# Kernel optimization log

Measured on AMD Instinct MI355X. Metric: run time of the kernel, lower is better.

Reference implementation:

```python
import jax, jax.numpy as jnp
import numpy as np

EPS = 1e-5  # nn.BatchNorm2d default eps
K = 3       # number of adjacency subsets


def setup_inputs() -> dict:
    key = jax.random.key(0)
    ks = jax.random.split(key, 8)
    N, C, T, V = 64, 64, 256, 25
    Cout = 64
    x = jax.random.normal(ks[0], (N, C, T, V), dtype=jnp.float32)
    A = jax.random.uniform(ks[1], (K, V, V), dtype=jnp.float32) * 0.1  # normalized-ish adjacency
    PA = jnp.ones((K, V, V), dtype=jnp.float32)  # torch.ones_like(A) init
    Wc = jax.random.normal(ks[2], (K * Cout, C), dtype=jnp.float32) * 0.05  # 1x1 conv weight
    bc = jax.random.normal(ks[3], (K * Cout,), dtype=jnp.float32) * 0.01
    gamma = 0.5 + jax.random.uniform(ks[4], (Cout,), dtype=jnp.float32)
    beta = jax.random.normal(ks[5], (Cout,), dtype=jnp.float32) * 0.1
    mean = jax.random.normal(ks[6], (Cout,), dtype=jnp.float32) * 0.1
    var = 0.5 + jax.random.uniform(ks[7], (Cout,), dtype=jnp.float32)
    return {"x": x, "A": A, "PA": PA, "Wc": Wc, "bc": bc,
            "gamma": gamma, "beta": beta, "mean": mean, "var": var}


def reference(x, A, PA, Wc, bc, gamma, beta, mean, var):
    # x: (n, c, t, v). in_channels == out_channels -> residual is identity.
    n, c, t, v = x.shape
    res = x
    Aeff = A * PA  # (k, v, w)
    # 1x1 conv: (n,c,t,v) x (o,c) -> (n,o,t,v), o = K*Cout
    y = jnp.einsum('nctv,oc->notv', x, Wc) + bc[None, :, None, None]
    cout = y.shape[1] // K
    y = y.reshape(n, K, cout, t, v)
    # per-subset graph aggregation: (n,k,c,t,v) x (k,v,w) -> (n,c,t,w)
    z = jnp.einsum('nkctv,kvw->nctw', y, Aeff)
    # BatchNorm2d (eval mode) over channel dim
    inv = jax.lax.rsqrt(var + EPS)
    bn = (z - mean[None, :, None, None]) * (gamma * inv)[None, :, None, None] + beta[None, :, None, None]
    return jax.nn.relu(bn + res)
```

## Files before the change

### kernel.cpp

```cpp
#include <hip/hip_runtime.h>
#include <hip/hip_bf16.h>

typedef __attribute__((ext_vector_type(8))) short short8;
typedef __attribute__((ext_vector_type(4))) float floatx4;
typedef __attribute__((ext_vector_type(4))) unsigned short ushortx4;

#define TT 4
#define XS_PITCH 136

#define WS_W2 0
#define WS_AE 24576
#define WS_F  30720
#define WS_S  38912

__device__ __forceinline__ float bf2f(unsigned short u) {
    return __uint_as_float(((unsigned int)u) << 16);
}
__device__ __forceinline__ unsigned short f2bf(float f) {
    unsigned int xx = __float_as_uint(f);
    return (unsigned short)((xx + 0x7fffu + ((xx >> 16) & 1u)) >> 16);
}

__global__ __launch_bounds__(256) void gcn_prep(
    const float* __restrict__ A, const float* __restrict__ PA,
    const float* __restrict__ Wc, const float* __restrict__ bc,
    const float* __restrict__ gamma_, const float* __restrict__ beta_,
    const float* __restrict__ mean_, const float* __restrict__ var_,
    unsigned short* __restrict__ w2, unsigned short* __restrict__ ae,
    float* __restrict__ Fx, float* __restrict__ sarr)
{
    const int b = blockIdx.x, tid = threadIdx.x;
    if (b == 0) {
        __shared__ float cs[96];
        if (tid < 96) {
            int k = tid >> 5, w = tid & 31;
            float s = 0.f;
            if (w < 25)
                for (int v = 0; v < 25; ++v) {
                    int ai = (k * 25 + v) * 25 + w;
                    s += A[ai] * PA[ai];
                }
            cs[tid] = s;
        }
        if (tid < 64) sarr[tid] = gamma_[tid] * rsqrtf(var_[tid] + 1e-5f);
        __syncthreads();
        for (int e = tid; e < 2048; e += 256) {
            int w = e >> 6, co = e & 63;
            float val = 0.f;
            if (w < 25) {
                float sc = gamma_[co] * rsqrtf(var_[co] + 1e-5f);
                val = beta_[co] - mean_[co] * sc
                    + sc * (bc[co] * cs[w] + bc[64 + co] * cs[32 + w] + bc[128 + co] * cs[64 + w]);
            }
            Fx[e] = val;
        }
    } else if (b == 1) {
        for (int e = tid; e < 3072; e += 256) {
            int k = e >> 10, r = e & 1023, w = r >> 5, v = r & 31;
            unsigned short val = 0;
            if (v < 25 && w < 25) {
                int ai = (k * 25 + v) * 25 + w;
                val = f2bf(A[ai] * PA[ai]);
            }
            ae[e] = val;
        }
    } else {
        const int half = b - 2;
        for (int e = tid + half * 6144; e < (half + 1) * 6144; e += 256) {
            int co = e / 192, kc = e % 192, k = kc >> 6, c = kc & 63;
            w2[e] = f2bf(Wc[(k * 64 + co) * 64 + c]);
        }
    }
}

__global__ __launch_bounds__(256, 4) void gcn_main(
    const float* __restrict__ x,
    const unsigned short* __restrict__ w2g,
    const unsigned short* __restrict__ aeg,
    const float* __restrict__ Fg,
    const float* __restrict__ sg,
    float* __restrict__ out)
{
#if defined(__gfx950__)
    __shared__ __align__(16) unsigned short Xs[64 * XS_PITCH];
    __shared__ __align__(16) unsigned short XAbuf[4 * 2 * 1024];

    const int tid = threadIdx.x;
    const int n  = blockIdx.x >> 6;
    const int t0 = (blockIdx.x & 63) * TT;
    const float* xn = x + (size_t)n * 409600;

    {
        const int c = tid >> 2, tl = tid & 3;
        const float* gp = xn + (c * 256 + t0 + tl) * 25;
        unsigned short* dst = &Xs[c * XS_PITCH + tl * 32];
        float f[32];
#pragma unroll
        for (int j = 0; j < 25; ++j) f[j] = gp[j];
#pragma unroll
        for (int j = 25; j < 32; ++j) f[j] = 0.f;
#pragma unroll
        for (int vc = 0; vc < 4; ++vc) {
            union { short8 v; unsigned short s[8]; } u;
#pragma unroll
            for (int j = 0; j < 8; ++j) u.s[j] = f2bf(f[vc * 8 + j]);
            *(short8*)&dst[vc * 8] = u.v;
        }
    }

    const int wave = tid >> 6, lane = tid & 63;
    const int l15 = lane & 15, quad = lane >> 4;
    const int t = wave;

    short8 aeffB[3][2];
#pragma unroll
    for (int k = 0; k < 3; ++k)
#pragma unroll
        for (int nt = 0; nt < 2; ++nt)
            aeffB[k][nt] = *(const short8*)&aeg[(k * 32 + nt * 16 + l15) * 32 + quad * 8];

    __syncthreads();

    unsigned short* xa = &XAbuf[wave * 2048];
    const int wlo3 = l15 & 3, qh = quad >> 1, ql = quad & 1;
    const int woff00 = (l15     ) * 64 + (((0 + qh) ^ wlo3) << 4) + ql * 8;
    const int woff01 = (16 + l15) * 64 + (((0 + qh) ^ wlo3) << 4) + ql * 8;
    const int woff10 = (l15     ) * 64 + (((2 + qh) ^ wlo3) << 4) + ql * 8;
    const int woff11 = (16 + l15) * 64 + (((2 + qh) ^ wlo3) << 4) + ql * 8;
    const int roff0  = (l15     ) * 64 + ((quad ^ wlo3) << 4);
    const int roff1  = (16 + l15) * 64 + ((quad ^ wlo3) << 4);

    const floatx4 zero4 = {0.f, 0.f, 0.f, 0.f};
    floatx4 zacc[4][2];
#pragma unroll
    for (int ct = 0; ct < 4; ++ct) { zacc[ct][0] = zero4; zacc[ct][1] = zero4; }

    const unsigned short* xsrow = &Xs[t * 32 + quad * 8];

#pragma unroll
    for (int ch = 0; ch < 6; ++ch) {
        const int k = ch >> 1, cc = ch & 1;
        char* xab = (char*)xa + (ch & 1) * 2048;

        short8 xf0 = *(const short8*)&xsrow[(cc * 32      + l15) * XS_PITCH];
        short8 xf1 = *(const short8*)&xsrow[(cc * 32 + 16 + l15) * XS_PITCH];
        floatx4 d00 = __builtin_amdgcn_mfma_f32_16x16x32_bf16(xf0, aeffB[k][0], zero4, 0, 0, 0);
        floatx4 d01 = __builtin_amdgcn_mfma_f32_16x16x32_bf16(xf0, aeffB[k][1], zero4, 0, 0, 0);
        floatx4 d10 = __builtin_amdgcn_mfma_f32_16x16x32_bf16(xf1, aeffB[k][0], zero4, 0, 0, 0);
        floatx4 d11 = __builtin_amdgcn_mfma_f32_16x16x32_bf16(xf1, aeffB[k][1], zero4, 0, 0, 0);

        {
            ushortx4 p;
            p[0] = f2bf(d00[0]); p[1] = f2bf(d00[1]); p[2] = f2bf(d00[2]); p[3] = f2bf(d00[3]);
            *(ushortx4*)(xab + woff00) = p;
            p[0] = f2bf(d01[0]); p[1] = f2bf(d01[1]); p[2] = f2bf(d01[2]); p[3] = f2bf(d01[3]);
            *(ushortx4*)(xab + woff01) = p;
            p[0] = f2bf(d10[0]); p[1] = f2bf(d10[1]); p[2] = f2bf(d10[2]); p[3] = f2bf(d10[3]);
            *(ushortx4*)(xab + woff10) = p;
            p[0] = f2bf(d11[0]); p[1] = f2bf(d11[1]); p[2] = f2bf(d11[2]); p[3] = f2bf(d11[3]);
            *(ushortx4*)(xab + woff11) = p;
        }

        short8 b0 = *(const short8*)(xab + roff0);
        short8 b1 = *(const short8*)(xab + roff1);
        const unsigned short* wrow = &w2g[l15 * 192 + k * 64 + cc * 32 + quad * 8];
#pragma unroll
        for (int ct = 0; ct < 4; ++ct) {
            short8 wf = *(const short8*)&wrow[ct * 16 * 192];
            zacc[ct][0] = __builtin_amdgcn_mfma_f32_16x16x32_bf16(wf, b0, zacc[ct][0], 0, 0, 0);
            zacc[ct][1] = __builtin_amdgcn_mfma_f32_16x16x32_bf16(wf, b1, zacc[ct][1], 0, 0, 0);
        }
    }

    const unsigned short* resp = &Xs[(quad * 4) * XS_PITCH + t * 32 + l15];
    float* outp = out + ((size_t)(n * 64 + quad * 4) * 256 + t0 + t) * 25 + l15;
#pragma unroll
    for (int ct = 0; ct < 4; ++ct) {
        floatx4 sv = *(const floatx4*)&sg[ct * 16 + quad * 4];
#pragma unroll
        for (int wt = 0; wt < 2; ++wt) {
            floatx4 Fv = *(const floatx4*)&Fg[(wt * 16 + l15) * 64 + ct * 16 + quad * 4];
            if (wt == 0 || l15 < 9) {
#pragma unroll
                for (int r = 0; r < 4; ++r) {
                    float xres = bf2f(resp[(ct * 16 + r) * XS_PITCH + wt * 16]);
                    float val = sv[r] * zacc[ct][wt][r] + Fv[r] + xres;
                    outp[(size_t)(ct * 16 + r) * 6400 + wt * 16] = fmaxf(val, 0.f);
                }
            }
        }
    }
#else
    (void)x; (void)w2g; (void)aeg; (void)Fg; (void)sg; (void)out;
#endif
}

extern "C" void kernel_launch(void* const* d_in, const int* in_sizes, int n_in,
                              void* d_out, int out_size, void* d_ws, size_t ws_size,
                              hipStream_t stream) {
    (void)in_sizes; (void)n_in; (void)out_size; (void)ws_size;
    unsigned short* w2 = (unsigned short*)((char*)d_ws + WS_W2);
    unsigned short* ae = (unsigned short*)((char*)d_ws + WS_AE);
    float*          Fx = (float*)((char*)d_ws + WS_F);
    float*          sa = (float*)((char*)d_ws + WS_S);

    gcn_prep<<<dim3(4), dim3(256), 0, stream>>>(
        (const float*)d_in[1], (const float*)d_in[2], (const float*)d_in[3],
        (const float*)d_in[4], (const float*)d_in[5], (const float*)d_in[6],
        (const float*)d_in[7], (const float*)d_in[8], w2, ae, Fx, sa);

    gcn_main<<<dim3(64 * 64), dim3(256), 0, stream>>>(
        (const float*)d_in[0], w2, ae, Fx, sa, (float*)d_out);
}
```

Measured before the change: 270.8 us.

## Process eight timesteps per block with XOR-swizzled LDS and per-output-column passes

Each block now covers 8 timesteps instead of 4, with each wave handling two timesteps, and the grid is halved. The X tile is stored in LDS with an XOR swizzle instead of padding. The output-vertex tiles (wt) are processed sequentially, so only one set of Aeff fragments and two accumulator sets live at once. The goal is to amortise weight and Aeff loads across more timesteps and cut register pressure, at the cost of fewer blocks, more LDS per block (which may lower occupancy), and a serial loop over wt.

```diff
diff --git a/kernel.cpp b/kernel.cpp
--- a/kernel.cpp
+++ b/kernel.cpp
@@ -4,9 +4,6 @@
 typedef __attribute__((ext_vector_type(8))) short short8;
 typedef __attribute__((ext_vector_type(4))) float floatx4;
 typedef __attribute__((ext_vector_type(4))) unsigned short ushortx4;
-
-#define TT 4
-#define XS_PITCH 136
 
 #define WS_W2 0
 #define WS_AE 24576
@@ -82,110 +79,116 @@
     float* __restrict__ out)
 {
 #if defined(__gfx950__)
-    __shared__ __align__(16) unsigned short Xs[64 * XS_PITCH];
-    __shared__ __align__(16) unsigned short XAbuf[4 * 2 * 1024];
+    __shared__ __align__(16) unsigned short Xs[64 * 256];
+    __shared__ __align__(16) unsigned short XAbuf[8 * 512];
 
     const int tid = threadIdx.x;
-    const int n  = blockIdx.x >> 6;
-    const int t0 = (blockIdx.x & 63) * TT;
+    const int n  = blockIdx.x >> 5;
+    const int t0 = (blockIdx.x & 31) * 8;
     const float* xn = x + (size_t)n * 409600;
 
-    {
-        const int c = tid >> 2, tl = tid & 3;
-        const float* gp = xn + (c * 256 + t0 + tl) * 25;
-        unsigned short* dst = &Xs[c * XS_PITCH + tl * 32];
+#pragma unroll
+    for (int i = 0; i < 2; ++i) {
+        const int idx = tid + i * 256;
+        const int c = idx >> 3, t = idx & 7;
+        const float* gp = xn + (c * 256 + t0 + t) * 25;
         float f[32];
 #pragma unroll
         for (int j = 0; j < 25; ++j) f[j] = gp[j];
 #pragma unroll
         for (int j = 25; j < 32; ++j) f[j] = 0.f;
+        unsigned short* base = &Xs[c * 256];
+        const int sw = c & 7;
 #pragma unroll
         for (int vc = 0; vc < 4; ++vc) {
             union { short8 v; unsigned short s[8]; } u;
 #pragma unroll
             for (int j = 0; j < 8; ++j) u.s[j] = f2bf(f[vc * 8 + j]);
-            *(short8*)&dst[vc * 8] = u.v;
+            *(short8*)&base[(((t * 4 + vc) ^ sw)) * 8] = u.v;
         }
     }
+    __syncthreads();
 
     const int wave = tid >> 6, lane = tid & 63;
     const int l15 = lane & 15, quad = lane >> 4;
-    const int t = wave;
-
-    short8 aeffB[3][2];
-#pragma unroll
-    for (int k = 0; k < 3; ++k)
-#pragma unroll
-        for (int nt = 0; nt < 2; ++nt)
-            aeffB[k][nt] = *(const short8*)&aeg[(k * 32 + nt * 16 + l15) * 32 + quad * 8];
-
-    __syncthreads();
-
-    unsigned short* xa = &XAbuf[wave * 2048];
+    const int tA = wave * 2, tB = wave * 2 + 1;
+    const int swf = l15 & 7;
+
+    unsigned short* bufA = &XAbuf[(wave * 2 + 0) * 512];
+    unsigned short* bufB = &XAbuf[(wave * 2 + 1) * 512];
     const int wlo3 = l15 & 3, qh = quad >> 1, ql = quad & 1;
-    const int woff00 = (l15     ) * 64 + (((0 + qh) ^ wlo3) << 4) + ql * 8;
-    const int woff01 = (16 + l15) * 64 + (((0 + qh) ^ wlo3) << 4) + ql * 8;
-    const int woff10 = (l15     ) * 64 + (((2 + qh) ^ wlo3) << 4) + ql * 8;
-    const int woff11 = (16 + l15) * 64 + (((2 + qh) ^ wlo3) << 4) + ql * 8;
-    const int roff0  = (l15     ) * 64 + ((quad ^ wlo3) << 4);
-    const int roff1  = (16 + l15) * 64 + ((quad ^ wlo3) << 4);
+    const int woff0 = l15 * 32 + ((qh ^ wlo3) << 3) + (ql << 2);
+    const int woff1 = l15 * 32 + (((2 + qh) ^ wlo3) << 3) + (ql << 2);
+    const int roff  = l15 * 32 + ((quad ^ wlo3) << 3);
 
     const floatx4 zero4 = {0.f, 0.f, 0.f, 0.f};
-    floatx4 zacc[4][2];
-#pragma unroll
-    for (int ct = 0; ct < 4; ++ct) { zacc[ct][0] = zero4; zacc[ct][1] = zero4; }
-
-    const unsigned short* xsrow = &Xs[t * 32 + quad * 8];
-
-#pragma unroll
-    for (int ch = 0; ch < 6; ++ch) {
-        const int k = ch >> 1, cc = ch & 1;
-        char* xab = (char*)xa + (ch & 1) * 2048;
-
-        short8 xf0 = *(const short8*)&xsrow[(cc * 32      + l15) * XS_PITCH];
-        short8 xf1 = *(const short8*)&xsrow[(cc * 32 + 16 + l15) * XS_PITCH];
-        floatx4 d00 = __builtin_amdgcn_mfma_f32_16x16x32_bf16(xf0, aeffB[k][0], zero4, 0, 0, 0);
-        floatx4 d01 = __builtin_amdgcn_mfma_f32_16x16x32_bf16(xf0, aeffB[k][1], zero4, 0, 0, 0);
-        floatx4 d10 = __builtin_amdgcn_mfma_f32_16x16x32_bf16(xf1, aeffB[k][0], zero4, 0, 0, 0);
-        floatx4 d11 = __builtin_amdgcn_mfma_f32_16x16x32_bf16(xf1, aeffB[k][1], zero4, 0, 0, 0);
-
-        {
-            ushortx4 p;
-            p[0] = f2bf(d00[0]); p[1] = f2bf(d00[1]); p[2] = f2bf(d00[2]); p[3] = f2bf(d00[3]);
-            *(ushortx4*)(xab + woff00) = p;
-            p[0] = f2bf(d01[0]); p[1] = f2bf(d01[1]); p[2] = f2bf(d01[2]); p[3] = f2bf(d01[3]);
-            *(ushortx4*)(xab + woff01) = p;
-            p[0] = f2bf(d10[0]); p[1] = f2bf(d10[1]); p[2] = f2bf(d10[2]); p[3] = f2bf(d10[3]);
-            *(ushortx4*)(xab + woff10) = p;
-            p[0] = f2bf(d11[0]); p[1] = f2bf(d11[1]); p[2] = f2bf(d11[2]); p[3] = f2bf(d11[3]);
-            *(ushortx4*)(xab + woff11) = p;
-        }
-
-        short8 b0 = *(const short8*)(xab + roff0);
-        short8 b1 = *(const short8*)(xab + roff1);
-        const unsigned short* wrow = &w2g[l15 * 192 + k * 64 + cc * 32 + quad * 8];
-#pragma unroll
-        for (int ct = 0; ct < 4; ++ct) {
-            short8 wf = *(const short8*)&wrow[ct * 16 * 192];
-            zacc[ct][0] = __builtin_amdgcn_mfma_f32_16x16x32_bf16(wf, b0, zacc[ct][0], 0, 0, 0);
-            zacc[ct][1] = __builtin_amdgcn_mfma_f32_16x16x32_bf16(wf, b1, zacc[ct][1], 0, 0, 0);
-        }
-    }
-
-    const unsigned short* resp = &Xs[(quad * 4) * XS_PITCH + t * 32 + l15];
-    float* outp = out + ((size_t)(n * 64 + quad * 4) * 256 + t0 + t) * 25 + l15;
-#pragma unroll
-    for (int ct = 0; ct < 4; ++ct) {
-        floatx4 sv = *(const floatx4*)&sg[ct * 16 + quad * 4];
-#pragma unroll
-        for (int wt = 0; wt < 2; ++wt) {
-            floatx4 Fv = *(const floatx4*)&Fg[(wt * 16 + l15) * 64 + ct * 16 + quad * 4];
-            if (wt == 0 || l15 < 9) {
-#pragma unroll
-                for (int r = 0; r < 4; ++r) {
-                    float xres = bf2f(resp[(ct * 16 + r) * XS_PITCH + wt * 16]);
-                    float val = sv[r] * zacc[ct][wt][r] + Fv[r] + xres;
-                    outp[(size_t)(ct * 16 + r) * 6400 + wt * 16] = fmaxf(val, 0.f);
+
+#pragma unroll 1
+    for (int wt = 0; wt < 2; ++wt) {
+        short8 aeff[3];
+#pragma unroll
+        for (int k = 0; k < 3; ++k)
+            aeff[k] = *(const short8*)&aeg[(k * 32 + wt * 16 + l15) * 32 + quad * 8];
+
+        floatx4 zA[4], zB[4];
+#pragma unroll
+        for (int ct = 0; ct < 4; ++ct) { zA[ct] = zero4; zB[ct] = zero4; }
+
+#pragma unroll
+        for (int ch = 0; ch < 6; ++ch) {
+            const int k = ch >> 1, cc = ch & 1;
+            const int c0 = cc * 32 + l15, c1 = cc * 32 + 16 + l15;
+
+            short8 x0A = *(const short8*)&Xs[c0 * 256 + ((tA * 4 + quad) ^ swf) * 8];
+            short8 x1A = *(const short8*)&Xs[c1 * 256 + ((tA * 4 + quad) ^ swf) * 8];
+            short8 x0B = *(const short8*)&Xs[c0 * 256 + ((tB * 4 + quad) ^ swf) * 8];
+            short8 x1B = *(const short8*)&Xs[c1 * 256 + ((tB * 4 + quad) ^ swf) * 8];
+            floatx4 dA0 = __builtin_amdgcn_mfma_f32_16x16x32_bf16(x0A, aeff[k], zero4, 0, 0, 0);
+            floatx4 dA1 = __builtin_amdgcn_mfma_f32_16x16x32_bf16(x1A, aeff[k], zero4, 0, 0, 0);
+            floatx4 dB0 = __builtin_amdgcn_mfma_f32_16x16x32_bf16(x0B, aeff[k], zero4, 0, 0, 0);
+            floatx4 dB1 = __builtin_amdgcn_mfma_f32_16x16x32_bf16(x1B, aeff[k], zero4, 0, 0, 0);
+
+            {
+                ushortx4 p;
+                p[0] = f2bf(dA0[0]); p[1] = f2bf(dA0[1]); p[2] = f2bf(dA0[2]); p[3] = f2bf(dA0[3]);
+                *(ushortx4*)&bufA[woff0] = p;
+                p[0] = f2bf(dA1[0]); p[1] = f2bf(dA1[1]); p[2] = f2bf(dA1[2]); p[3] = f2bf(dA1[3]);
+                *(ushortx4*)&bufA[woff1] = p;
+                p[0] = f2bf(dB0[0]); p[1] = f2bf(dB0[1]); p[2] = f2bf(dB0[2]); p[3] = f2bf(dB0[3]);
+                *(ushortx4*)&bufB[woff0] = p;
+                p[0] = f2bf(dB1[0]); p[1] = f2bf(dB1[1]); p[2] = f2bf(dB1[2]); p[3] = f2bf(dB1[3]);
+                *(ushortx4*)&bufB[woff1] = p;
+            }
+
+            short8 bA = *(const short8*)&bufA[roff];
+            short8 bB = *(const short8*)&bufB[roff];
+
+            const unsigned short* wrow = &w2g[l15 * 192 + k * 64 + cc * 32 + quad * 8];
+#pragma unroll
+            for (int ct = 0; ct < 4; ++ct) {
+                short8 wf = *(const short8*)&wrow[ct * 16 * 192];
+                zA[ct] = __builtin_amdgcn_mfma_f32_16x16x32_bf16(wf, bA, zA[ct], 0, 0, 0);
+                zB[ct] = __builtin_amdgcn_mfma_f32_16x16x32_bf16(wf, bB, zB[ct], 0, 0, 0);
+            }
+        }
+
+        const int w = wt * 16 + l15;
+        if (wt == 0 || l15 < 9) {
+#pragma unroll
+            for (int tc = 0; tc < 2; ++tc) {
+                const int t = (tc == 0) ? tA : tB;
+                const floatx4* z = (tc == 0) ? zA : zB;
+#pragma unroll
+                for (int ct = 0; ct < 4; ++ct) {
+                    floatx4 sv = *(const floatx4*)&sg[ct * 16 + quad * 4];
+                    floatx4 Fv = *(const floatx4*)&Fg[w * 64 + ct * 16 + quad * 4];
+#pragma unroll
+                    for (int r = 0; r < 4; ++r) {
+                        const int co = ct * 16 + quad * 4 + r;
+                        float xres = bf2f(Xs[co * 256 + (((t * 4 + (w >> 3)) ^ (co & 7)) * 8) + (w & 7)]);
+                        float val = sv[r] * z[ct][r] + Fv[r] + xres;
+                        out[((size_t)(n * 64 + co) * 256 + t0 + t) * 25 + w] = fmaxf(val, 0.f);
+                    }
                 }
             }
         }
@@ -209,6 +212,6 @@
         (const float*)d_in[4], (const float*)d_in[5], (const float*)d_in[6],
         (const float*)d_in[7], (const float*)d_in[8], w2, ae, Fx, sa);
 
-    gcn_main<<<dim3(64 * 64), dim3(256), 0, stream>>>(
+    gcn_main<<<dim3(64 * 32), dim3(256), 0, stream>>>(
         (const float*)d_in[0], w2, ae, Fx, sa, (float*)d_out);
 }
```

New measurement: 422.7 us. 56.1% more time.

## Stage x via coalesced float4 loads and cache W2 in LDS with swizzle

Applied to the files above, without the earlier changes.

The input tile is first loaded with coalesced float4 reads into an LDS staging area, then converted to bf16 into an XOR-swizzled layout that replaces the padded pitch. The conv weight matrix W2 is copied into padded LDS once per block instead of being read from global memory inside the MFMA loop. The per-wave XA buffer becomes single-buffered and reuses the staging region. LDS use rises to about 49KB and launch bounds drop to 3 blocks per SM, which may reduce occupancy and adds two extra barriers.

```diff
diff --git a/kernel.cpp b/kernel.cpp
--- a/kernel.cpp
+++ b/kernel.cpp
@@ -4,9 +4,6 @@
 typedef __attribute__((ext_vector_type(8))) short short8;
 typedef __attribute__((ext_vector_type(4))) float floatx4;
 typedef __attribute__((ext_vector_type(4))) unsigned short ushortx4;
-
-#define TT 4
-#define XS_PITCH 136
 
 #define WS_W2 0
 #define WS_AE 24576
@@ -73,7 +70,7 @@
     }
 }
 
-__global__ __launch_bounds__(256, 4) void gcn_main(
+__global__ __launch_bounds__(256, 3) void gcn_main(
     const float* __restrict__ x,
     const unsigned short* __restrict__ w2g,
     const unsigned short* __restrict__ aeg,
@@ -82,21 +79,43 @@
     float* __restrict__ out)
 {
 #if defined(__gfx950__)
-    __shared__ __align__(16) unsigned short Xs[64 * XS_PITCH];
-    __shared__ __align__(16) unsigned short XAbuf[4 * 2 * 1024];
+    __shared__ __align__(16) unsigned char LB[50176];
+    unsigned short* Xs  = (unsigned short*)LB;
+    unsigned short* XA  = (unsigned short*)(LB + 16384);
+    unsigned short* W2s = (unsigned short*)(LB + 24576);
+    float*          T   = (float*)(LB + 16384);
 
     const int tid = threadIdx.x;
     const int n  = blockIdx.x >> 6;
-    const int t0 = (blockIdx.x & 63) * TT;
+    const int t0 = (blockIdx.x & 63) * 4;
     const float* xn = x + (size_t)n * 409600;
 
+    const int wave = tid >> 6, lane = tid & 63;
+    const int l15 = lane & 15, quad = lane >> 4;
+
+    short8 aeff[3][2];
+#pragma unroll
+    for (int k = 0; k < 3; ++k)
+#pragma unroll
+        for (int nt = 0; nt < 2; ++nt)
+            aeff[k][nt] = *(const short8*)&aeg[(k * 32 + nt * 16 + l15) * 32 + quad * 8];
+
+#pragma unroll
+    for (int i = 0; i < 7; ++i) {
+        int q = tid + (i << 8);
+        if (q < 1600) {
+            int c = q / 25, j = q % 25;
+            *(floatx4*)&T[q * 4] = *(const floatx4*)&xn[c * 6400 + t0 * 25 + j * 4];
+        }
+    }
+    __syncthreads();
+
     {
-        const int c = tid >> 2, tl = tid & 3;
-        const float* gp = xn + (c * 256 + t0 + tl) * 25;
-        unsigned short* dst = &Xs[c * XS_PITCH + tl * 32];
+        const int c = tid >> 2, tl = tid & 3, key = c & 7;
+        const float* tr = &T[c * 100 + tl * 25];
         float f[32];
 #pragma unroll
-        for (int j = 0; j < 25; ++j) f[j] = gp[j];
+        for (int j = 0; j < 25; ++j) f[j] = tr[j];
 #pragma unroll
         for (int j = 25; j < 32; ++j) f[j] = 0.f;
 #pragma unroll
@@ -104,50 +123,48 @@
             union { short8 v; unsigned short s[8]; } u;
 #pragma unroll
             for (int j = 0; j < 8; ++j) u.s[j] = f2bf(f[vc * 8 + j]);
-            *(short8*)&dst[vc * 8] = u.v;
-        }
-    }
-
-    const int wave = tid >> 6, lane = tid & 63;
-    const int l15 = lane & 15, quad = lane >> 4;
+            *(short8*)&Xs[c * 128 + (((tl * 4 + vc) ^ key) << 3)] = u.v;
+        }
+    }
+    __syncthreads();
+
+    {
+        const int co = tid >> 2, g = tid & 3;
+#pragma unroll
+        for (int jj = 0; jj < 6; ++jj) {
+            int j = g * 6 + jj;
+            *(short8*)&W2s[co * 200 + j * 8] = *(const short8*)&w2g[co * 192 + j * 8];
+        }
+    }
+    __syncthreads();
+
     const int t = wave;
-
-    short8 aeffB[3][2];
-#pragma unroll
-    for (int k = 0; k < 3; ++k)
-#pragma unroll
-        for (int nt = 0; nt < 2; ++nt)
-            aeffB[k][nt] = *(const short8*)&aeg[(k * 32 + nt * 16 + l15) * 32 + quad * 8];
-
-    __syncthreads();
-
-    unsigned short* xa = &XAbuf[wave * 2048];
+    char* xab = (char*)XA + wave * 2048;
     const int wlo3 = l15 & 3, qh = quad >> 1, ql = quad & 1;
-    const int woff00 = (l15     ) * 64 + (((0 + qh) ^ wlo3) << 4) + ql * 8;
-    const int woff01 = (16 + l15) * 64 + (((0 + qh) ^ wlo3) << 4) + ql * 8;
-    const int woff10 = (l15     ) * 64 + (((2 + qh) ^ wlo3) << 4) + ql * 8;
+    const int woff00 = l15 * 64        + ((qh ^ wlo3) << 4) + ql * 8;
+    const int woff01 = (16 + l15) * 64 + ((qh ^ wlo3) << 4) + ql * 8;
+    const int woff10 = l15 * 64        + (((2 + qh) ^ wlo3) << 4) + ql * 8;
     const int woff11 = (16 + l15) * 64 + (((2 + qh) ^ wlo3) << 4) + ql * 8;
-    const int roff0  = (l15     ) * 64 + ((quad ^ wlo3) << 4);
+    const int roff0  = l15 * 64        + ((quad ^ wlo3) << 4);
     const int roff1  = (16 + l15) * 64 + ((quad ^ wlo3) << 4);
+    const int xoffX  = ((t * 4 + quad) ^ (l15 & 7)) << 3;
 
     const floatx4 zero4 = {0.f, 0.f, 0.f, 0.f};
     floatx4 zacc[4][2];
 #pragma unroll
     for (int ct = 0; ct < 4; ++ct) { zacc[ct][0] = zero4; zacc[ct][1] = zero4; }
 
-    const unsigned short* xsrow = &Xs[t * 32 + quad * 8];
-
 #pragma unroll
     for (int ch = 0; ch < 6; ++ch) {
         const int k = ch >> 1, cc = ch & 1;
-        char* xab = (char*)xa + (ch & 1) * 2048;
-
-        short8 xf0 = *(const short8*)&xsrow[(cc * 32      + l15) * XS_PITCH];
-        short8 xf1 = *(const short8*)&xsrow[(cc * 32 + 16 + l15) * XS_PITCH];
-        floatx4 d00 = __builtin_amdgcn_mfma_f32_16x16x32_bf16(xf0, aeffB[k][0], zero4, 0, 0, 0);
-        floatx4 d01 = __builtin_amdgcn_mfma_f32_16x16x32_bf16(xf0, aeffB[k][1], zero4, 0, 0, 0);
-        floatx4 d10 = __builtin_amdgcn_mfma_f32_16x16x32_bf16(xf1, aeffB[k][0], zero4, 0, 0, 0);
-        floatx4 d11 = __builtin_amdgcn_mfma_f32_16x16x32_bf16(xf1, aeffB[k][1], zero4, 0, 0, 0);
+        const int c0 = cc * 32 + l15, c1 = c0 + 16;
+
+        short8 xf0 = *(const short8*)&Xs[c0 * 128 + xoffX];
+        short8 xf1 = *(const short8*)&Xs[c1 * 128 + xoffX];
+        floatx4 d00 = __builtin_amdgcn_mfma_f32_16x16x32_bf16(xf0, aeff[k][0], zero4, 0, 0, 0);
+        floatx4 d01 = __builtin_amdgcn_mfma_f32_16x16x32_bf16(xf0, aeff[k][1], zero4, 0, 0, 0);
+        floatx4 d10 = __builtin_amdgcn_mfma_f32_16x16x32_bf16(xf1, aeff[k][0], zero4, 0, 0, 0);
+        floatx4 d11 = __builtin_amdgcn_mfma_f32_16x16x32_bf16(xf1, aeff[k][1], zero4, 0, 0, 0);
 
         {
             ushortx4 p;
@@ -160,32 +177,31 @@
             p[0] = f2bf(d11[0]); p[1] = f2bf(d11[1]); p[2] = f2bf(d11[2]); p[3] = f2bf(d11[3]);
             *(ushortx4*)(xab + woff11) = p;
         }
-
         short8 b0 = *(const short8*)(xab + roff0);
         short8 b1 = *(const short8*)(xab + roff1);
-        const unsigned short* wrow = &w2g[l15 * 192 + k * 64 + cc * 32 + quad * 8];
+
 #pragma unroll
         for (int ct = 0; ct < 4; ++ct) {
-            short8 wf = *(const short8*)&wrow[ct * 16 * 192];
+            short8 wf = *(const short8*)&W2s[(ct * 16 + l15) * 200 + (k * 8 + cc * 4 + quad) * 8];
             zacc[ct][0] = __builtin_amdgcn_mfma_f32_16x16x32_bf16(wf, b0, zacc[ct][0], 0, 0, 0);
             zacc[ct][1] = __builtin_amdgcn_mfma_f32_16x16x32_bf16(wf, b1, zacc[ct][1], 0, 0, 0);
         }
     }
 
-    const unsigned short* resp = &Xs[(quad * 4) * XS_PITCH + t * 32 + l15];
-    float* outp = out + ((size_t)(n * 64 + quad * 4) * 256 + t0 + t) * 25 + l15;
-#pragma unroll
-    for (int ct = 0; ct < 4; ++ct) {
-        floatx4 sv = *(const floatx4*)&sg[ct * 16 + quad * 4];
-#pragma unroll
-        for (int wt = 0; wt < 2; ++wt) {
-            floatx4 Fv = *(const floatx4*)&Fg[(wt * 16 + l15) * 64 + ct * 16 + quad * 4];
-            if (wt == 0 || l15 < 9) {
+#pragma unroll
+    for (int wt = 0; wt < 2; ++wt) {
+        const int w = wt * 16 + l15;
+        if (wt == 0 || l15 < 9) {
+#pragma unroll
+            for (int ct = 0; ct < 4; ++ct) {
+                floatx4 sv = *(const floatx4*)&sg[ct * 16 + quad * 4];
+                floatx4 Fv = *(const floatx4*)&Fg[w * 64 + ct * 16 + quad * 4];
 #pragma unroll
                 for (int r = 0; r < 4; ++r) {
-                    float xres = bf2f(resp[(ct * 16 + r) * XS_PITCH + wt * 16]);
+                    const int co = ct * 16 + quad * 4 + r;
+                    float xres = bf2f(Xs[co * 128 + (((t * 4 + (w >> 3)) ^ (co & 7)) << 3) + (w & 7)]);
                     float val = sv[r] * zacc[ct][wt][r] + Fv[r] + xres;
-                    outp[(size_t)(ct * 16 + r) * 6400 + wt * 16] = fmaxf(val, 0.f);
+                    out[((size_t)(n * 64 + co) * 256 + t0 + t) * 25 + w] = fmaxf(val, 0.f);
                 }
             }
         }
```

New measurement: 252.0 us. -6.9%, faster.
